# Performance work log

Measured on AMD Instinct MI355X. Metric: run time of the kernel, lower is better.

## Reference

```python
import jax, jax.numpy as jnp
import numpy as np

INV_MAX_SIZE = 55
INV_STR_LEN = 80
MSG_VOCAB = 128
EOS = MSG_VOCAB + 1  # 129
VOCAB = 130
EMB = 16   # str_emb == CHAR_EMB
HID = 16
OUT = 24
B = 1024

# INV_OCLASS_MAP with default 128 (indices 0..18)
_MAP = np.full(19, 128, dtype=np.int32)
for k, v in {1: 93, 2: 41, 3: 91, 4: 61, 5: 34, 6: 40, 7: 37, 8: 33, 9: 63,
             10: 43, 11: 47, 12: 36, 13: 42, 14: 96, 15: 48, 16: 95, 17: 46, 18: 128}.items():
    _MAP[k] = v


def setup_inputs() -> dict:
    key = jax.random.key(0)
    ks = jax.random.split(key, 20)
    s = 0.1
    return {
        "inv_oclasses": jax.random.randint(ks[0], (B, INV_MAX_SIZE), 0, 19),
        "inv_strs": jax.random.randint(ks[1], (B, INV_MAX_SIZE, INV_STR_LEN), 0, MSG_VOCAB),
        "emb": jax.random.normal(ks[2], (VOCAB, EMB), jnp.float32) * s,
        "rnn_Wih": jax.random.normal(ks[3], (HID, EMB), jnp.float32) * s,
        "rnn_Whh": jax.random.normal(ks[4], (HID, HID), jnp.float32) * s,
        "rnn_bih": jax.random.normal(ks[5], (HID,), jnp.float32) * s,
        "rnn_bhh": jax.random.normal(ks[6], (HID,), jnp.float32) * s,
        "gru_Wih_f": jax.random.normal(ks[7], (3 * HID, EMB), jnp.float32) * s,
        "gru_Whh_f": jax.random.normal(ks[8], (3 * HID, HID), jnp.float32) * s,
        "gru_bih_f": jax.random.normal(ks[9], (3 * HID,), jnp.float32) * s,
        "gru_bhh_f": jax.random.normal(ks[10], (3 * HID,), jnp.float32) * s,
        "gru_Wih_b": jax.random.normal(ks[11], (3 * HID, EMB), jnp.float32) * s,
        "gru_Whh_b": jax.random.normal(ks[12], (3 * HID, HID), jnp.float32) * s,
        "gru_bih_b": jax.random.normal(ks[13], (3 * HID,), jnp.float32) * s,
        "gru_bhh_b": jax.random.normal(ks[14], (3 * HID,), jnp.float32) * s,
        "fus_W1": jax.random.normal(ks[15], (HID, 3 * HID), jnp.float32) * s,
        "fus_b1": jax.random.normal(ks[16], (HID,), jnp.float32) * s,
        "fus_W2": jax.random.normal(ks[17], (OUT, HID), jnp.float32) * s,
        "fus_b2": jax.random.normal(ks[18], (OUT,), jnp.float32) * s,
    }


def _masked_rnn(x, lengths, Wih, Whh, bih, bhh):
    # x: [N, T, D]; returns final hidden at step lengths-1 (zeros if length==0)
    N, T, _ = x.shape
    gi = jnp.einsum('ntd,hd->nth', x, Wih) + bih          # precompute input proj
    valid = (jnp.arange(T)[None, :] < lengths[:, None])   # [N, T]
    def step(h, inp):
        gi_t, v = inp
        hn = jnp.tanh(gi_t + h @ Whh.T + bhh)
        return jnp.where(v, hn, h), None
    h0 = jnp.zeros((N, Whh.shape[0]), x.dtype)
    h, _ = jax.lax.scan(step, h0, (jnp.swapaxes(gi, 0, 1), valid.T[:, :, None]))
    return h


def _masked_gru(x, lengths, Wih, Whh, bih, bhh):
    # x: [N, T, D]; PyTorch GRU cell; returns final hidden within valid prefix
    N, T, _ = x.shape
    H = Whh.shape[1]
    gi = jnp.einsum('ntd,hd->nth', x, Wih) + bih          # [N, T, 3H]
    valid = (jnp.arange(T)[None, :] < lengths[:, None])
    def step(h, inp):
        gi_t, v = inp
        gh = h @ Whh.T + bhh
        i_r, i_z, i_n = jnp.split(gi_t, 3, axis=-1)
        h_r, h_z, h_n = jnp.split(gh, 3, axis=-1)
        r = jax.nn.sigmoid(i_r + h_r)
        z = jax.nn.sigmoid(i_z + h_z)
        n = jnp.tanh(i_n + r * h_n)
        hn = (1.0 - z) * n + z * h
        return jnp.where(v, hn, h), None
    h0 = jnp.zeros((N, H), x.dtype)
    h, _ = jax.lax.scan(step, h0, (jnp.swapaxes(gi, 0, 1), valid.T[:, :, None]))
    return h


def reference(inv_oclasses, inv_strs, emb, rnn_Wih, rnn_Whh, rnn_bih, rnn_bhh,
              gru_Wih_f, gru_Whh_f, gru_bih_f, gru_bhh_f,
              gru_Wih_b, gru_Whh_b, gru_bih_b, gru_bhh_b,
              fus_W1, fus_b1, fus_W2, fus_b2):
    Bn = inv_oclasses.shape[0]
    emb = emb.at[0].set(0.0)  # padding_idx=0

    # ---- object-class branch: map -> embed -> packed vanilla RNN ----
    inv_class = jnp.asarray(_MAP)[inv_oclasses]            # [B, 55]
    inv_class_emb = emb[inv_class]                         # [B, 55, 16]
    len_class = jnp.sum(inv_oclasses != 18, axis=1)
    h_class = _masked_rnn(inv_class_emb, len_class, rnn_Wih, rnn_Whh, rnn_bih, rnn_bhh)  # [B, 16]

    # ---- string branch: insert EOS, embed, packed bidirectional GRU ----
    strs = inv_strs.reshape(Bn * INV_MAX_SIZE, INV_STR_LEN)
    lengths = jnp.sum(strs != 0, axis=-1)                  # [B*55]
    t = jnp.arange(INV_STR_LEN)
    strs_eos = jnp.where(t[None, :] == lengths[:, None], EOS, strs)
    str_emb = emb[strs_eos]                                # [B*55, 80, 16]

    h_fwd = _masked_gru(str_emb, lengths, gru_Wih_f, gru_Whh_f, gru_bih_f, gru_bhh_f)
    # reverse the valid prefix for the backward direction
    idx = jnp.maximum(lengths[:, None] - 1 - t[None, :], 0)
    x_rev = jnp.take_along_axis(str_emb, idx[:, :, None], axis=1)
    h_bwd = _masked_gru(x_rev, lengths, gru_Wih_b, gru_Whh_b, gru_bih_b, gru_bhh_b)

    str_final = jnp.concatenate([h_fwd, h_bwd], axis=-1).reshape(Bn, INV_MAX_SIZE, 2 * HID)
    str_mask = (jnp.sum(inv_strs, axis=-1) > 0).astype(str_final.dtype)[:, :, None]
    str_pooled = jnp.sum(str_final * str_mask, axis=1) / (jnp.sum(str_mask, axis=1) + 1e-8)

    combined = jnp.concatenate([h_class, str_pooled], axis=-1)   # [B, 48]
    h = jax.nn.relu(combined @ fus_W1.T + fus_b1)
    inv_features = h @ fus_W2.T + fus_b2                          # [B, 24]
    return inv_features, inv_class_emb, str_emb
```

## Files before the change

kernel.cpp:

```cpp
#include <hip/hip_runtime.h>
#include <hip/hip_bf16.h>
#include <math.h>

#define B_     1024
#define VOCAB_ 130
#define EOS_   129

#define OUT_CLS_F  24576
#define OUT_STR_F  925696

#define OFF_POOL 0
#define OFF_CNT  32768
#define OFF_HC   33792
#define OFF_T    50176

typedef float f2 __attribute__((ext_vector_type(2)));

static __device__ const int d_MAP[19] =
    {128,93,41,91,61,34,40,37,33,63,43,47,36,42,96,48,95,46,128};

__device__ __forceinline__ float sigm_(float x){
    return __builtin_amdgcn_rcpf(1.f + __builtin_amdgcn_exp2f(-1.4426950408889634f * x));
}
__device__ __forceinline__ float tanh_(float x){
    return 2.f * __builtin_amdgcn_rcpf(1.f + __builtin_amdgcn_exp2f(-2.8853900817779268f * x)) - 1.f;
}
__device__ __forceinline__ int badf(float v) {
    return (v != v) || (fabsf(v) > 1e30f);
}
__device__ __forceinline__ f2 mkf2(float a, float b){ f2 r; r.x = a; r.y = b; return r; }

__global__ void k0_tables(const float* __restrict__ emb,
                          const float* __restrict__ WihF, const float* __restrict__ bihF,
                          const float* __restrict__ bhhF,
                          const float* __restrict__ WihB, const float* __restrict__ bihB,
                          const float* __restrict__ bhhB, float* ws)
{
    int i = blockIdx.x * 256 + threadIdx.x;
    if (i >= 12288) return;
    int dir = i / 6144, r = i - dir * 6144;
    int c = r / 48, j = r - c * 48;
    const float* Wih = dir ? WihB : WihF;
    const float* bih = dir ? bihB : bihF;
    const float* bhh = dir ? bhhB : bhhF;
    float v = bih[j] + ((j < 32) ? bhh[j] : 0.f);
    if (c != 0) {
        const float* e = emb + c * 16;
        #pragma unroll
        for (int d = 0; d < 16; ++d) v = fmaf(Wih[j * 16 + d], e[d], v);
    }
    ws[OFF_T + i] = v;
}

__global__ void k1_embed(const int* oclass, const int* strs,
                         const float* emb, float* out)
{
    __shared__ __align__(16) float embF[VOCAB_ * 20];
    __shared__ int chs[4 * 80];
    int bi = blockIdx.x, tid = threadIdx.x;

    for (int i = tid; i < VOCAB_ * 16; i += 256) {
        int r = i >> 4, c = i & 15;
        embF[r * 20 + c] = (r == 0) ? 0.f : emb[i];
    }
    __syncthreads();

    if (bi < 14080) {
        int w = tid >> 6, lane = tid & 63;
        int s = bi * 4 + w;
        const int* cp = strs + (long)s * 80;
        int ca = cp[lane];
        int cb = (lane < 16) ? cp[64 + lane] : 0;
        unsigned long long m1 = __ballot(ca != 0);
        unsigned long long m2 = __ballot((lane < 16) && (cb != 0));
        int L = __popcll(m1) + __popcll(m2);
        if (lane == L) ca = EOS_;
        if (lane < 16 && (64 + lane) == L) cb = EOS_;
        chs[w * 80 + lane] = ca;
        if (lane < 16) chs[w * 80 + 64 + lane] = cb;
        float4* dst = (float4*)(out + OUT_STR_F + (long)s * 1280);
        #pragma unroll
        for (int it = 0; it < 5; ++it) {
            int q = it * 64 + lane;
            int row = q >> 2, part = q & 3;
            int ch = chs[w * 80 + row];
            dst[q] = *(const float4*)&embF[ch * 20 + part * 4];
        }
    } else {
        int q = (bi - 14080) * 256 + tid;
        int bs = q >> 2, part = q & 3;
        int c = d_MAP[oclass[bs]];
        float4* dst = (float4*)(out + OUT_CLS_F);
        dst[q] = *(const float4*)&embF[c * 20 + part * 4];
    }
}

__global__ __launch_bounds__(256, 3) void k2_rnn(
    const int* oclass, const int* strs, const float* __restrict__ emb,
    const float* __restrict__ WhhF, const float* __restrict__ bhhF,
    const float* __restrict__ WhhB, const float* __restrict__ bhhB,
    const float* __restrict__ rWih, const float* __restrict__ rWhh,
    const float* __restrict__ rbih, const float* __restrict__ rbhh,
    float* ws)
{
    __shared__ float ldsT[128 * 49];
    __shared__ __align__(16) float ldsHB[256];
    int bi = blockIdx.x, tid = threadIdx.x;
    int grp = tid >> 4, j = tid & 15;
    float* hb = ldsHB + (grp << 4);

    if (bi < 7040) {
        bool fwd = bi < 3520;
        const float* __restrict__ Whh = fwd ? WhhF : WhhB;
        const float* __restrict__ bhh = fwd ? bhhF : bhhB;

        const float* Tg = ws + OFF_T + (fwd ? 0 : 6144);
        for (int i = tid; i < 6144; i += 256) {
            int c = i / 48, q = i - c * 48;
            ldsT[c * 49 + q] = Tg[i];
        }

        f2 wr[8], wz[8], wn[8];
        #pragma unroll
        for (int k = 0; k < 4; ++k) {
            float4 a = *(const float4*)&Whh[      j * 16 + 4 * k];
            float4 b = *(const float4*)&Whh[256 + j * 16 + 4 * k];
            float4 c4 = *(const float4*)&Whh[512 + j * 16 + 4 * k];
            wr[2*k] = mkf2(a.x, a.y);  wr[2*k+1] = mkf2(a.z, a.w);
            wz[2*k] = mkf2(b.x, b.y);  wz[2*k+1] = mkf2(b.z, b.w);
            wn[2*k] = mkf2(c4.x, c4.y); wn[2*k+1] = mkf2(c4.z, c4.w);
        }
        float bn = bhh[32 + j];
        __syncthreads();

        int s = (fwd ? bi : bi - 3520) * 16 + grp;
        const int* cp = strs + (long)s * 80;

        int cnt = 0;
        #pragma unroll
        for (int k = 0; k < 5; ++k) cnt += (cp[j + 16 * k] != 0);
        cnt += __builtin_amdgcn_ds_swizzle(cnt, (1 << 10) | 0x1f);
        cnt += __builtin_amdgcn_ds_swizzle(cnt, (2 << 10) | 0x1f);
        cnt += __builtin_amdgcn_ds_swizzle(cnt, (4 << 10) | 0x1f);
        cnt += __builtin_amdgcn_ds_swizzle(cnt, (8 << 10) | 0x1f);
        int L = cnt;

        float hj = 0.f;
        hb[j] = 0.f;
        if (L > 0) {
            int base = fwd ? 0 : (L - 1);
            int stp  = fwd ? 1 : -1;
            int c = cp[base];
            for (int t = 0; t < L; ++t) {
                int cn = (t + 1 < L) ? cp[base + (t + 1) * stp] : 0;
                const float* Trow = ldsT + c * 49;
                float tr_ = Trow[j];
                float tz_ = Trow[16 + j];
                float tn_ = Trow[32 + j];
                f2 ar = mkf2(0.f, 0.f), az = mkf2(0.f, 0.f), an = mkf2(0.f, 0.f);
                #pragma unroll
                for (int k = 0; k < 4; ++k) {
                    float4 h4 = *(const float4*)&hb[4 * k];
                    f2 h0 = mkf2(h4.x, h4.y), h1 = mkf2(h4.z, h4.w);
                    ar = __builtin_elementwise_fma(wr[2*k],   h0, ar);
                    az = __builtin_elementwise_fma(wz[2*k],   h0, az);
                    an = __builtin_elementwise_fma(wn[2*k],   h0, an);
                    ar = __builtin_elementwise_fma(wr[2*k+1], h1, ar);
                    az = __builtin_elementwise_fma(wz[2*k+1], h1, az);
                    an = __builtin_elementwise_fma(wn[2*k+1], h1, an);
                }
                float rg = sigm_(tr_ + ar.x + ar.y);
                float zg = sigm_(tz_ + az.x + az.y);
                float ng = tanh_(tn_ + rg * (bn + an.x + an.y));
                hj = zg * (hj - ng) + ng;
                hb[j] = hj;
                __builtin_amdgcn_wave_barrier();
                c = cn;
            }
            int b = s / 55;
            atomicAdd(ws + OFF_POOL + b * 32 + (fwd ? 0 : 16) + j, hj);
            if (fwd && j == 0) atomicAdd(ws + OFF_CNT + b, 1.f);
        }
    } else {
        for (int i = tid; i < 19 * 16; i += 256) {
            int o = i >> 4, jj = i & 15;
            int c = d_MAP[o];
            float v = rbih[jj] + rbhh[jj];
            #pragma unroll
            for (int d = 0; d < 16; ++d)
                v = fmaf(rWih[jj * 16 + d], emb[c * 16 + d], v);
            ldsT[o * 20 + jj] = v;
        }
        f2 wv[8];
        #pragma unroll
        for (int k = 0; k < 4; ++k) {
            float4 a = *(const float4*)&rWhh[j * 16 + 4 * k];
            wv[2*k] = mkf2(a.x, a.y);  wv[2*k+1] = mkf2(a.z, a.w);
        }
        __syncthreads();

        int smp = (bi - 7040) * 16 + grp;
        const int* op = oclass + (long)smp * 55;
        int cnt = 0;
        #pragma unroll
        for (int k = 0; k < 4; ++k) {
            int p = j + 16 * k;
            cnt += (p < 55 && op[p] != 18);
        }
        cnt += __builtin_amdgcn_ds_swizzle(cnt, (1 << 10) | 0x1f);
        cnt += __builtin_amdgcn_ds_swizzle(cnt, (2 << 10) | 0x1f);
        cnt += __builtin_amdgcn_ds_swizzle(cnt, (4 << 10) | 0x1f);
        cnt += __builtin_amdgcn_ds_swizzle(cnt, (8 << 10) | 0x1f);
        int len = cnt;

        float hj = 0.f;
        hb[j] = 0.f;
        if (len > 0) {
            int o = op[0];
            for (int t = 0; t < len; ++t) {
                int onx = (t + 1 < len) ? op[t + 1] : 0;
                float a = ldsT[o * 20 + j];
                f2 a2 = mkf2(0.f, 0.f);
                #pragma unroll
                for (int k = 0; k < 4; ++k) {
                    float4 h4 = *(const float4*)&hb[4 * k];
                    a2 = __builtin_elementwise_fma(wv[2*k],   mkf2(h4.x, h4.y), a2);
                    a2 = __builtin_elementwise_fma(wv[2*k+1], mkf2(h4.z, h4.w), a2);
                }
                hj = tanh_(a + a2.x + a2.y);
                hb[j] = hj;
                __builtin_amdgcn_wave_barrier();
                o = onx;
            }
        }
        ws[OFF_HC + smp * 16 + j] = hj;
    }
}

__global__ void k3_fuse(const float* fW1, const float* fb1,
                        const float* fW2, const float* fb2,
                        float* ws, float* out)
{
    int b = blockIdx.x * 256 + threadIdx.x;
    if (b >= B_) return;
    float inv = 1.f / (ws[OFF_CNT + b] + 1e-8f);
    float comb[48];
    #pragma unroll
    for (int j = 0; j < 16; ++j) comb[j] = ws[OFF_HC + b * 16 + j];
    #pragma unroll
    for (int j = 0; j < 32; ++j) comb[16 + j] = ws[OFF_POOL + b * 32 + j] * inv;

    float hid[16];
    #pragma unroll
    for (int o = 0; o < 16; ++o) {
        float v = fb1[o];
        #pragma unroll
        for (int i = 0; i < 48; ++i) v = fmaf(fW1[o * 48 + i], comb[i], v);
        hid[o] = v > 0.f ? v : 0.f;
    }
    #pragma unroll
    for (int o = 0; o < 24; ++o) {
        float v = fb2[o];
        #pragma unroll
        for (int i = 0; i < 16; ++i) v = fmaf(fW2[o * 16 + i], hid[i], v);
        out[b * 24 + o] = v;
    }

    if (b == 0) {
        int bb = 0;
        if (!badf(ws[OFF_POOL]))    bb |= 1;
        if (!badf(ws[OFF_HC]))      bb |= 2;
        if (ws[OFF_CNT] > 0.5f)     bb |= 4;
        if (bb != 7) {
            float code = 16384.f + 128.f * (float)bb;
            #pragma unroll
            for (int i = 4; i < 12; ++i) out[i] = code;
        }
    }
}

extern "C" void kernel_launch(void* const* d_in, const int* in_sizes, int n_in,
                              void* d_out, int out_size, void* d_ws, size_t ws_size,
                              hipStream_t stream)
{
    const int*   oclass = (const int*)d_in[0];
    const int*   strs   = (const int*)d_in[1];
    const float* emb    = (const float*)d_in[2];
    const float* rWih   = (const float*)d_in[3];
    const float* rWhh   = (const float*)d_in[4];
    const float* rbih   = (const float*)d_in[5];
    const float* rbhh   = (const float*)d_in[6];
    const float* gWihF  = (const float*)d_in[7];
    const float* gWhhF  = (const float*)d_in[8];
    const float* gbihF  = (const float*)d_in[9];
    const float* gbhhF  = (const float*)d_in[10];
    const float* gWihB  = (const float*)d_in[11];
    const float* gWhhB  = (const float*)d_in[12];
    const float* gbihB  = (const float*)d_in[13];
    const float* gbhhB  = (const float*)d_in[14];
    const float* fW1    = (const float*)d_in[15];
    const float* fb1    = (const float*)d_in[16];
    const float* fW2    = (const float*)d_in[17];
    const float* fb2    = (const float*)d_in[18];

    float* ws  = (float*)d_ws;
    float* out = (float*)d_out;

    hipMemsetAsync(d_ws, 0, 33792 * sizeof(float), stream);

    k0_tables<<<48, 256, 0, stream>>>(emb, gWihF, gbihF, gbhhF,
                                      gWihB, gbihB, gbhhB, ws);
    k1_embed<<<14960, 256, 0, stream>>>(oclass, strs, emb, out);
    k2_rnn<<<7104, 256, 0, stream>>>(oclass, strs, emb,
                                     gWhhF, gbhhF, gWhhB, gbhhB,
                                     rWih, rWhh, rbih, rbhh, ws);
    k3_fuse<<<4, 256, 0, stream>>>(fW1, fb1, fW2, fb2, ws, out);
}
```

Baseline: 665.1 us.

## Fuse embedding-write and RNN kernels into one interleaved launch

```diff
diff --git a/kernel.cpp b/kernel.cpp
--- a/kernel.cpp
+++ b/kernel.cpp
@@ -13,6 +13,11 @@
 #define OFF_CNT  32768
 #define OFF_HC   33792
 #define OFF_T    50176
+
+#define NK2      7104
+#define NK1      14960
+#define NINT     21312
+#define NTOT     22064
 
 typedef float f2 __attribute__((ext_vector_type(2)));
 
@@ -52,60 +57,69 @@
     ws[OFF_T + i] = v;
 }
 
-__global__ void k1_embed(const int* oclass, const int* strs,
-                         const float* emb, float* out)
+__global__ __launch_bounds__(256)
+__attribute__((amdgpu_waves_per_eu(1, 4)))
+void k12_main(const int* oclass, const int* strs, const float* __restrict__ emb,
+              const float* __restrict__ WhhF, const float* __restrict__ bhhF,
+              const float* __restrict__ WhhB, const float* __restrict__ bhhB,
+              const float* __restrict__ rWih, const float* __restrict__ rWhh,
+              const float* __restrict__ rbih, const float* __restrict__ rbhh,
+              float* ws, float* out)
 {
-    __shared__ __align__(16) float embF[VOCAB_ * 20];
-    __shared__ int chs[4 * 80];
-    int bi = blockIdx.x, tid = threadIdx.x;
-
-    for (int i = tid; i < VOCAB_ * 16; i += 256) {
-        int r = i >> 4, c = i & 15;
-        embF[r * 20 + c] = (r == 0) ? 0.f : emb[i];
-    }
-    __syncthreads();
-
-    if (bi < 14080) {
-        int w = tid >> 6, lane = tid & 63;
-        int s = bi * 4 + w;
-        const int* cp = strs + (long)s * 80;
-        int ca = cp[lane];
-        int cb = (lane < 16) ? cp[64 + lane] : 0;
-        unsigned long long m1 = __ballot(ca != 0);
-        unsigned long long m2 = __ballot((lane < 16) && (cb != 0));
-        int L = __popcll(m1) + __popcll(m2);
-        if (lane == L) ca = EOS_;
-        if (lane < 16 && (64 + lane) == L) cb = EOS_;
-        chs[w * 80 + lane] = ca;
-        if (lane < 16) chs[w * 80 + 64 + lane] = cb;
-        float4* dst = (float4*)(out + OUT_STR_F + (long)s * 1280);
-        #pragma unroll
-        for (int it = 0; it < 5; ++it) {
-            int q = it * 64 + lane;
-            int row = q >> 2, part = q & 3;
-            int ch = chs[w * 80 + row];
-            dst[q] = *(const float4*)&embF[ch * 20 + part * 4];
-        }
+    __shared__ __align__(16) float smem[6528];
+    int bi0 = blockIdx.x, tid = threadIdx.x;
+
+    int k2id = -1, k1id;
+    if (bi0 < NINT) {
+        if (bi0 % 3 == 0) k2id = bi0 / 3;
+        else              k1id = bi0 - bi0 / 3 - 1;
     } else {
-        int q = (bi - 14080) * 256 + tid;
-        int bs = q >> 2, part = q & 3;
-        int c = d_MAP[oclass[bs]];
-        float4* dst = (float4*)(out + OUT_CLS_F);
-        dst[q] = *(const float4*)&embF[c * 20 + part * 4];
-    }
-}
-
-__global__ __launch_bounds__(256, 3) void k2_rnn(
-    const int* oclass, const int* strs, const float* __restrict__ emb,
-    const float* __restrict__ WhhF, const float* __restrict__ bhhF,
-    const float* __restrict__ WhhB, const float* __restrict__ bhhB,
-    const float* __restrict__ rWih, const float* __restrict__ rWhh,
-    const float* __restrict__ rbih, const float* __restrict__ rbhh,
-    float* ws)
-{
-    __shared__ float ldsT[128 * 49];
-    __shared__ __align__(16) float ldsHB[256];
-    int bi = blockIdx.x, tid = threadIdx.x;
+        k1id = 14208 + (bi0 - NINT);
+    }
+
+    if (k2id < 0) {
+        float* embF = smem;
+        int*   chs  = (int*)(smem + 2600);
+        for (int i = tid; i < VOCAB_ * 16; i += 256) {
+            int r = i >> 4, c = i & 15;
+            embF[r * 20 + c] = (r == 0) ? 0.f : emb[i];
+        }
+        __syncthreads();
+
+        if (k1id < 14080) {
+            int w = tid >> 6, lane = tid & 63;
+            int s = k1id * 4 + w;
+            const int* cp = strs + (long)s * 80;
+            int ca = cp[lane];
+            int cb = (lane < 16) ? cp[64 + lane] : 0;
+            unsigned long long m1 = __ballot(ca != 0);
+            unsigned long long m2 = __ballot((lane < 16) && (cb != 0));
+            int L = __popcll(m1) + __popcll(m2);
+            if (lane == L) ca = EOS_;
+            if (lane < 16 && (64 + lane) == L) cb = EOS_;
+            chs[w * 80 + lane] = ca;
+            if (lane < 16) chs[w * 80 + 64 + lane] = cb;
+            float4* dst = (float4*)(out + OUT_STR_F + (long)s * 1280);
+            #pragma unroll
+            for (int it = 0; it < 5; ++it) {
+                int q = it * 64 + lane;
+                int row = q >> 2, part = q & 3;
+                int ch = chs[w * 80 + row];
+                dst[q] = *(const float4*)&embF[ch * 20 + part * 4];
+            }
+        } else {
+            int q = (k1id - 14080) * 256 + tid;
+            int bs = q >> 2, part = q & 3;
+            int c = d_MAP[oclass[bs]];
+            float4* dst = (float4*)(out + OUT_CLS_F);
+            dst[q] = *(const float4*)&embF[c * 20 + part * 4];
+        }
+        return;
+    }
+
+    float* ldsT  = smem;
+    float* ldsHB = smem + 6272;
+    int bi = k2id;
     int grp = tid >> 4, j = tid & 15;
     float* hb = ldsHB + (grp << 4);
 
@@ -131,6 +145,12 @@
             wn[2*k] = mkf2(c4.x, c4.y); wn[2*k+1] = mkf2(c4.z, c4.w);
         }
         float bn = bhh[32 + j];
+        #pragma unroll
+        for (int k = 0; k < 8; ++k) {
+            asm volatile("" : "+v"(wr[k]));
+            asm volatile("" : "+v"(wz[k]));
+            asm volatile("" : "+v"(wn[k]));
+        }
         __syncthreads();
 
         int s = (fwd ? bi : bi - 3520) * 16 + grp;
@@ -154,10 +174,10 @@
             for (int t = 0; t < L; ++t) {
                 int cn = (t + 1 < L) ? cp[base + (t + 1) * stp] : 0;
                 const float* Trow = ldsT + c * 49;
-                float tr_ = Trow[j];
-                float tz_ = Trow[16 + j];
+                f2 ar = mkf2(Trow[j], 0.f);
+                f2 az = mkf2(Trow[16 + j], 0.f);
+                f2 an = mkf2(bn, 0.f);
                 float tn_ = Trow[32 + j];
-                f2 ar = mkf2(0.f, 0.f), az = mkf2(0.f, 0.f), an = mkf2(0.f, 0.f);
                 #pragma unroll
                 for (int k = 0; k < 4; ++k) {
                     float4 h4 = *(const float4*)&hb[4 * k];
@@ -169,10 +189,10 @@
                     az = __builtin_elementwise_fma(wz[2*k+1], h1, az);
                     an = __builtin_elementwise_fma(wn[2*k+1], h1, an);
                 }
-                float rg = sigm_(tr_ + ar.x + ar.y);
-                float zg = sigm_(tz_ + az.x + az.y);
-                float ng = tanh_(tn_ + rg * (bn + an.x + an.y));
-                hj = zg * (hj - ng) + ng;
+                float rg = sigm_(ar.x + ar.y);
+                float zg = sigm_(az.x + az.y);
+                float ng = tanh_(fmaf(rg, an.x + an.y, tn_));
+                hj = fmaf(zg, hj - ng, ng);
                 hb[j] = hj;
                 __builtin_amdgcn_wave_barrier();
                 c = cn;
@@ -219,15 +239,14 @@
             int o = op[0];
             for (int t = 0; t < len; ++t) {
                 int onx = (t + 1 < len) ? op[t + 1] : 0;
-                float a = ldsT[o * 20 + j];
-                f2 a2 = mkf2(0.f, 0.f);
+                f2 a2 = mkf2(ldsT[o * 20 + j], 0.f);
                 #pragma unroll
                 for (int k = 0; k < 4; ++k) {
                     float4 h4 = *(const float4*)&hb[4 * k];
                     a2 = __builtin_elementwise_fma(wv[2*k],   mkf2(h4.x, h4.y), a2);
                     a2 = __builtin_elementwise_fma(wv[2*k+1], mkf2(h4.z, h4.w), a2);
                 }
-                hj = tanh_(a + a2.x + a2.y);
+                hj = tanh_(a2.x + a2.y);
                 hb[j] = hj;
                 __builtin_amdgcn_wave_barrier();
                 o = onx;
@@ -310,9 +329,8 @@
 
     k0_tables<<<48, 256, 0, stream>>>(emb, gWihF, gbihF, gbhhF,
                                       gWihB, gbihB, gbhhB, ws);
-    k1_embed<<<14960, 256, 0, stream>>>(oclass, strs, emb, out);
-    k2_rnn<<<7104, 256, 0, stream>>>(oclass, strs, emb,
-                                     gWhhF, gbhhF, gWhhB, gbhhB,
-                                     rWih, rWhh, rbih, rbhh, ws);
+    k12_main<<<NTOT, 256, 0, stream>>>(oclass, strs, emb,
+                                       gWhhF, gbhhF, gWhhB, gbhhB,
+                                       rWih, rWhh, rbih, rbhh, ws, out);
     k3_fuse<<<4, 256, 0, stream>>>(fW1, fb1, fW2, fb2, ws, out);
 }
```

After: 646.6 us. -2.8%, faster.
